# Kernel optimization log

Hardware: AMD Instinct MI355X
Metric: run time of the kernel (lower is better)

Reference implementation:

```python
import jax, jax.numpy as jnp
import numpy as np

# ---- static config (matches init_kwargs cfg) ----
N_IMGS, C_FEAT = 9, 24
HF, WF = 112, 112            # quarter-res feature map
H_IMG, W_IMG = 448, 448      # CDR.IMG_SIZE
HD, WD = 56, 56              # DEPTH_PRED_SIZE
N_PLANES = 64                # DEPTH_MVS.N_INTERVALS
DEPTH_START, DEPTH_INTERVAL = 0.5, 0.05
EDGES_PER_REF = 8
N_EDGES = N_IMGS * EDGES_PER_REF
N_PIX = HD * WD


def setup_inputs() -> dict:
    key = jax.random.key(0)
    k1, k2, k3, k4 = jax.random.split(key, 4)
    feats_quarter = jax.random.normal(k1, (N_IMGS, C_FEAT, HF, WF), jnp.float32)
    # proper rotation matrices via QR so the camera math is well conditioned
    A = jax.random.normal(k2, (N_IMGS, 3, 3), jnp.float32)
    rotmats, _ = jnp.linalg.qr(A)
    rotmats = rotmats.astype(jnp.float32)
    tvecs = 0.1 * jax.random.normal(k3, (N_IMGS, 3), jnp.float32)
    K = jnp.broadcast_to(
        jnp.array([[400.0, 0.0, (W_IMG - 1) / 2.0],
                   [0.0, 400.0, (H_IMG - 1) / 2.0],
                   [0.0, 0.0, 1.0]], jnp.float32), (N_IMGS, 3, 3))
    # ref index sorted+repeated so unique(return_inverse) == ref row itself
    ref = jnp.repeat(jnp.arange(N_IMGS, dtype=jnp.int32), EDGES_PER_REF)
    src = jax.random.randint(k4, (N_EDGES,), 0, N_IMGS, dtype=jnp.int32)
    ref_src_edges = jnp.stack([ref, src], 0)
    return {"feats_quarter": feats_quarter, "rotmats": rotmats,
            "tvecs": tvecs, "K": K, "ref_src_edges": ref_src_edges}


def _forward(feats_quarter, rotmats, tvecs, K, ref_src_edges):
    ref_e, src_e = ref_src_edges[0], ref_src_edges[1]

    # ---- batched_build_plane_sweep_volume_tensor: world-space points per ref view ----
    us = jnp.linspace(0.0, W_IMG - 1.0, WD)
    vs = jnp.linspace(0.0, H_IMG - 1.0, HD)
    uu, vv = jnp.meshgrid(us, vs)                              # [HD, WD]
    pix = jnp.stack([uu, vv, jnp.ones_like(uu)], 0).reshape(3, N_PIX)
    rays = jnp.einsum('nij,jp->nip', jnp.linalg.inv(K), pix)  # [N, 3, P]
    depths = DEPTH_START + DEPTH_INTERVAL * jnp.arange(N_PLANES, dtype=jnp.float32)
    pts_cam = rays[:, None] * depths[None, :, None, None]      # [N, D, 3, P] (plane-major)
    pts_cam = pts_cam.transpose(0, 2, 1, 3).reshape(N_IMGS, 3, N_PLANES * N_PIX)
    pts_world = jnp.einsum('nji,njp->nip', rotmats, pts_cam - tvecs[:, :, None])
    n_pts = N_PLANES * N_PIX

    # ---- project ref-volume points into each src view (per edge) ----
    pts_homo = jnp.concatenate([pts_world, jnp.ones((N_IMGS, 1, n_pts), jnp.float32)], 1)
    P = jnp.einsum('nij,njk->nik', K, jnp.concatenate([rotmats, tvecs[:, :, None]], 2))  # [N,3,4]
    proj = jnp.einsum('eij,ejp->eip', P[src_e], pts_homo[ref_e])  # [E, 3, n_pts]
    z = jnp.abs(proj[:, 2]) + 1e-8
    gx = proj[:, 0] / z / (W_IMG - 1.0) * 2.0 - 1.0
    gy = proj[:, 1] / z / (H_IMG - 1.0) * 2.0 - 1.0

    # ---- bilinear grid_sample, align_corners=True, zeros padding ----
    def sample_one(img, gx1, gy1):  # img [C,HF,WF], gx1/gy1 [n_pts]
        x = (gx1 + 1.0) * 0.5 * (WF - 1)
        y = (gy1 + 1.0) * 0.5 * (HF - 1)
        x0 = jnp.floor(x)
        y0 = jnp.floor(y)
        wx1 = x - x0
        wy1 = y - y0

        def tap(xi, yi, w):
            valid = (xi >= 0) & (xi <= WF - 1) & (yi >= 0) & (yi <= HF - 1)
            xc = jnp.clip(xi, 0, WF - 1).astype(jnp.int32)
            yc = jnp.clip(yi, 0, HF - 1).astype(jnp.int32)
            return jnp.where(valid, w, 0.0)[None] * img[:, yc, xc]  # [C, n_pts]

        return (tap(x0, y0, (1 - wx1) * (1 - wy1))
                + tap(x0 + 1, y0, wx1 * (1 - wy1))
                + tap(x0, y0 + 1, (1 - wx1) * wy1)
                + tap(x0 + 1, y0 + 1, wx1 * wy1))

    x_vox = jax.vmap(sample_one)(feats_quarter[src_e], gx, gy)   # [E, C, n_pts]
    x_vox = x_vox.reshape(N_EDGES, C_FEAT, N_PLANES, HD, WD)

    # ---- scatter mean / sq-mean over edges sharing a ref image, then variance ----
    counts = jax.ops.segment_sum(jnp.ones((N_EDGES,), jnp.float32), ref_e, num_segments=N_IMGS)
    denom = jnp.maximum(counts, 1.0)[:, None, None, None, None]
    x_avg = jax.ops.segment_sum(x_vox, ref_e, num_segments=N_IMGS) / denom
    x_avg_sq = jax.ops.segment_sum(x_vox ** 2, ref_e, num_segments=N_IMGS) / denom
    return x_avg_sq - x_avg ** 2  # [n_ref, C, D, HD, WD]


def reference(feats_quarter, rotmats, tvecs, K, ref_src_edges):
    return _forward(feats_quarter, rotmats, tvecs, K, ref_src_edges)
```

## Files before the change

### kernel.cpp

```cpp
#include <hip/hip_runtime.h>

constexpr int kNImgs   = 9;
constexpr int kC       = 24;
constexpr int kHF      = 112, kWF = 112;
constexpr int kHD      = 56,  kWD = 56;
constexpr int kNPix    = kHD * kWD;
constexpr int kNPlanes = 64;
constexpr int kPtsPerRef = kNPlanes * kNPix;
constexpr int kEdgesPerRef = 8;
constexpr int kNEdges  = kNImgs * kEdgesPerRef;
constexpr int kFeatPix = kHF * kWF;
constexpr int kFeatPerImg = kC * kFeatPix;

constexpr int kDTile = 32, kPTile = 16;
constexpr int kDHalves = kNPlanes / kDTile;
constexpr int kPGroups = kNPix / kPTile;
constexpr int kBlocksPerRef = kDHalves * kPGroups;

typedef _Float16 half8  __attribute__((ext_vector_type(8)));
typedef _Float16 half2v __attribute__((ext_vector_type(2)));

#if __has_builtin(__builtin_amdgcn_fdot2)
__device__ inline float fdot2(half2v a, half2v b, float c) {
  return __builtin_amdgcn_fdot2(a, b, c, false);
}
#else
__device__ inline float fdot2(half2v a, half2v b, float c) {
  return c + (float)a[0] * (float)b[0] + (float)a[1] * (float)b[1];
}
#endif

__device__ inline void mm3(const float* A, const float* B, float* C) {
#pragma unroll
  for (int i = 0; i < 3; ++i)
#pragma unroll
    for (int j = 0; j < 3; ++j)
      C[i*3+j] = A[i*3+0]*B[0*3+j] + A[i*3+1]*B[1*3+j] + A[i*3+2]*B[2*3+j];
}

__device__ inline void inv3(const float* A, float* I) {
  float a=A[0],b=A[1],c=A[2],d=A[3],e=A[4],f=A[5],g=A[6],h=A[7],i=A[8];
  float c00 = e*i - f*h;
  float c01 = -(d*i - f*g);
  float c02 = d*h - e*g;
  float det = a*c00 + b*c01 + c*c02;
  float r = 1.0f / det;
  I[0] = c00*r;           I[1] = (c*h - b*i)*r;  I[2] = (b*f - c*e)*r;
  I[3] = c01*r;           I[4] = (a*i - c*g)*r;  I[5] = (c*d - a*f)*r;
  I[6] = c02*r;           I[7] = (b*g - a*h)*r;  I[8] = (a*e - b*d)*r;
}

__global__ __launch_bounds__(256)
void transpose_feats_kernel(const float* __restrict__ f, _Float16* __restrict__ ft) {
  int idx = blockIdx.x * 256 + threadIdx.x;
  if (idx >= kNImgs * kFeatPerImg) return;
  int n  = idx / kFeatPerImg;
  int r  = idx - n * kFeatPerImg;
  int c  = r / kFeatPix;
  int yx = r - c * kFeatPix;
  ft[((size_t)n * kFeatPix + yx) * kC + c] = (_Float16)f[idx];
}

template <bool TR>
__global__ __launch_bounds__(512)
void psv_var_kernel(const float* __restrict__ feats,
                    const _Float16* __restrict__ featsT,
                    const float* __restrict__ rotmats,
                    const float* __restrict__ tvecs,
                    const float* __restrict__ Kmat,
                    const int*   __restrict__ edges,
                    float* __restrict__ out) {
  __shared__ float sM[kEdgesPerRef][9];
  __shared__ float sB[kEdgesPerRef][3];
  __shared__ int   sSrc[kEdgesPerRef];
  __shared__ int   sUIdx[kEdgesPerRef];
  __shared__ float sMult[kEdgesPerRef];
  __shared__ int   sKU;
  __shared__ float sT[4][kDTile][kPTile + 1];

  const int nwg = gridDim.x;
  const int orig = blockIdx.x;
  const int q = nwg >> 3, r8 = nwg & 7;
  const int xcd = orig & 7, lin = orig >> 3;
  const int bid = ((xcd < r8) ? xcd * (q + 1) : r8 * (q + 1) + (xcd - r8) * q) + lin;

  const int n     = bid / kBlocksPerRef;
  const int rem   = bid - n * kBlocksPerRef;
  const int dHalf = rem / kPGroups;
  const int pG    = rem - dHalf * kPGroups;

  const int t = threadIdx.x;

  if (t < kEdgesPerRef) {
    const int e  = n * kEdgesPerRef + t;
    const int re = edges[e];
    const int se = edges[kNEdges + e];
    sSrc[t] = se;

    const float* Rr = rotmats + re * 9;
    const float* Rs = rotmats + se * 9;
    const float* Kr = Kmat + re * 9;
    const float* Ks = Kmat + se * 9;
    const float* tr = tvecs + re * 3;
    const float* ts = tvecs + se * 3;

    float RrT[9];
#pragma unroll
    for (int i = 0; i < 3; ++i)
#pragma unroll
      for (int j = 0; j < 3; ++j) RrT[i*3+j] = Rr[j*3+i];

    float Kinv[9], A[9], T1[9], M[9];
    inv3(Kr, Kinv);
    mm3(Rs, RrT, A);
    mm3(A, Kinv, T1);
    mm3(Ks, T1, M);

    float At0 = A[0]*tr[0] + A[1]*tr[1] + A[2]*tr[2];
    float At1 = A[3]*tr[0] + A[4]*tr[1] + A[5]*tr[2];
    float At2 = A[6]*tr[0] + A[7]*tr[1] + A[8]*tr[2];
    float bv0 = ts[0] - At0, bv1 = ts[1] - At1, bv2 = ts[2] - At2;
#pragma unroll
    for (int i = 0; i < 9; ++i) sM[t][i] = M[i];
#pragma unroll
    for (int i = 0; i < 3; ++i)
      sB[t][i] = Ks[i*3+0]*bv0 + Ks[i*3+1]*bv1 + Ks[i*3+2]*bv2;
  }
  __syncthreads();

  if (t == 0) {
    int k = 0;
    for (int j = 0; j < kEdgesPerRef; ++j) {
      const int s = sSrc[j];
      bool dup = false;
      for (int i = 0; i < k; ++i) {
        if (sSrc[sUIdx[i]] == s) { sMult[i] += 1.0f; dup = true; break; }
      }
      if (!dup) { sUIdx[k] = j; sMult[k] = 1.0f; ++k; }
    }
    sKU = k;
  }
  __syncthreads();

  const int dsub = t & 31;
  const int psub = t >> 5;
  const int d = dHalf * kDTile + dsub;
  const int p = pG * kPTile + psub;
  const int h = p / kWD;
  const int w = p - h * kWD;

  const float u = (float)w * (447.0f / 55.0f);
  const float v = (float)h * (447.0f / 55.0f);
  const float depth = 0.5f + 0.05f * (float)d;

  float acc[kC], accsq[kC];
#pragma unroll
  for (int c = 0; c < kC; ++c) { acc[c] = 0.0f; accsq[c] = 0.0f; }

  const int kU = sKU;
#pragma unroll 2
  for (int jj = 0; jj < kU; ++jj) {
    const int j = sUIdx[jj];
    const float mult = sMult[jj];
    const float* M = sM[j];
    const float px = depth * (M[0]*u + M[1]*v + M[2]) + sB[j][0];
    const float py = depth * (M[3]*u + M[4]*v + M[5]) + sB[j][1];
    const float pz = depth * (M[6]*u + M[7]*v + M[8]) + sB[j][2];
    const float rz = 1.0f / (fabsf(pz) + 1e-8f);

    const float x = px * rz * (111.0f / 447.0f);
    const float y = py * rz * (111.0f / 447.0f);

    const float x0 = floorf(x), y0 = floorf(y);
    const float wx = x - x0, wy = y - y0;
    const bool vx0 = (x0 >= 0.0f)  && (x0 <= 111.0f);
    const bool vx1 = (x0 >= -1.0f) && (x0 <= 110.0f);
    const bool vy0 = (y0 >= 0.0f)  && (y0 <= 111.0f);
    const bool vy1 = (y0 >= -1.0f) && (y0 <= 110.0f);
    const float w00 = (vx0 && vy0) ? (1.0f - wx) * (1.0f - wy) : 0.0f;
    const float w01 = (vx1 && vy0) ? wx * (1.0f - wy) : 0.0f;
    const float w10 = (vx0 && vy1) ? (1.0f - wx) * wy : 0.0f;
    const float w11 = (vx1 && vy1) ? wx * wy : 0.0f;

    const int xc0 = (int)fminf(fmaxf(x0,        0.0f), 111.0f);
    const int xc1 = (int)fminf(fmaxf(x0 + 1.0f, 0.0f), 111.0f);
    const int yc0 = (int)fminf(fmaxf(y0,        0.0f), 111.0f);
    const int yc1 = (int)fminf(fmaxf(y0 + 1.0f, 0.0f), 111.0f);

    const int src = sSrc[j];
    if constexpr (TR) {
      const half2v wr0 = {(_Float16)w00, (_Float16)w01};
      const half2v wr1 = {(_Float16)w10, (_Float16)w11};
      const _Float16* base = featsT + (size_t)src * kFeatPix * kC;
      const int o00 = (yc0 * kWF + xc0) * kC;
      const int o01 = (yc0 * kWF + xc1) * kC;
      const int o10 = (yc1 * kWF + xc0) * kC;
      const int o11 = (yc1 * kWF + xc1) * kC;
#pragma unroll
      for (int i = 0; i < kC / 8; ++i) {
        const half8 f00 = *(const half8*)(base + o00 + 8*i);
        const half8 f01 = *(const half8*)(base + o01 + 8*i);
        const half8 f10 = *(const half8*)(base + o10 + 8*i);
        const half8 f11 = *(const half8*)(base + o11 + 8*i);
#pragma unroll
        for (int k = 0; k < 8; ++k) {
          const half2v a0 = {f00[k], f01[k]};
          const half2v a1 = {f10[k], f11[k]};
          const float val = fdot2(a1, wr1, fdot2(a0, wr0, 0.0f));
          const int c = 8*i + k;
          const float mval = mult * val;
          acc[c] += mval;
          accsq[c] = __builtin_fmaf(mval, val, accsq[c]);
        }
      }
    } else {
      const float* base = feats + (size_t)src * kFeatPerImg;
      const int o00 = yc0 * kWF + xc0;
      const int o01 = yc0 * kWF + xc1;
      const int o10 = yc1 * kWF + xc0;
      const int o11 = yc1 * kWF + xc1;
#pragma unroll
      for (int c = 0; c < kC; ++c) {
        const float* bc = base + c * kFeatPix;
        float val = w00*bc[o00] + w01*bc[o01] + w10*bc[o10] + w11*bc[o11];
        const float mval = mult * val;
        acc[c] += mval;
        accsq[c] = __builtin_fmaf(mval, val, accsq[c]);
      }
    }
  }

  const int pp2 = t & (kPTile - 1);
  const int dd2 = t >> 4;
  const size_t outBase = (size_t)n * kC * (size_t)kPtsPerRef;
#pragma unroll
  for (int ch = 0; ch < kC / 4; ++ch) {
    __syncthreads();
#pragma unroll
    for (int cc = 0; cc < 4; ++cc) {
      const int c = ch * 4 + cc;
      const float mean = acc[c] * 0.125f;
      const float msq  = accsq[c] * 0.125f;
      sT[cc][dsub][psub] = msq - mean * mean;
    }
    __syncthreads();
#pragma unroll
    for (int cc = 0; cc < 4; ++cc) {
      const int c = ch * 4 + cc;
      out[outBase + ((size_t)c * kNPlanes + (dHalf * kDTile + dd2)) * kNPix
          + pG * kPTile + pp2] = sT[cc][dd2][pp2];
    }
  }
}

extern "C" void kernel_launch(void* const* d_in, const int* in_sizes, int n_in,
                              void* d_out, int out_size, void* d_ws, size_t ws_size,
                              hipStream_t stream) {
  const float* feats  = (const float*)d_in[0];
  const float* rot    = (const float*)d_in[1];
  const float* tv     = (const float*)d_in[2];
  const float* Kmat   = (const float*)d_in[3];
  const int*   edges  = (const int*)d_in[4];
  float* out = (float*)d_out;

  const size_t featsTBytes = (size_t)kNImgs * kFeatPix * kC * sizeof(_Float16);
  const int gridMain = kNImgs * kBlocksPerRef;

  if (ws_size >= featsTBytes) {
    _Float16* featsT = (_Float16*)d_ws;
    const int nT = kNImgs * kFeatPerImg;
    transpose_feats_kernel<<<(nT + 255) / 256, 256, 0, stream>>>(feats, featsT);
    psv_var_kernel<true><<<gridMain, 512, 0, stream>>>(feats, featsT, rot, tv, Kmat, edges, out);
  } else {
    psv_var_kernel<false><<<gridMain, 512, 0, stream>>>(feats, nullptr, rot, tv, Kmat, edges, out);
  }
}
```

Measured before the change: 155.7 us.

## Process both depth halves per thread with packed float2 accumulators

Each block now covers all 64 depth planes for its pixel group: every thread handles two depths (d and d+32). This halves the grid and reuses the per-edge projection terms (M·[u,v,1]) across both depths. Accumulators become float2 vectors so the mean and squared-mean updates can use packed FP32 ops, and the shared transpose tile is re-laid out to [p][d]. The cost is double the accumulator registers (96 floats), which may lower occupancy, plus fewer blocks to spread across the GPU.

Measured after the change: 191.2 us. 1.23x slower.

```diff
diff --git a/kernel.cpp b/kernel.cpp
--- a/kernel.cpp
+++ b/kernel.cpp
@@ -13,12 +13,12 @@
 constexpr int kFeatPerImg = kC * kFeatPix;
 
 constexpr int kDTile = 32, kPTile = 16;
-constexpr int kDHalves = kNPlanes / kDTile;
 constexpr int kPGroups = kNPix / kPTile;
-constexpr int kBlocksPerRef = kDHalves * kPGroups;
+constexpr int kBlocksPerRef = kPGroups;
 
 typedef _Float16 half8  __attribute__((ext_vector_type(8)));
 typedef _Float16 half2v __attribute__((ext_vector_type(2)));
+typedef float    float2v __attribute__((ext_vector_type(2)));
 
 #if __has_builtin(__builtin_amdgcn_fdot2)
 __device__ inline float fdot2(half2v a, half2v b, float c) {
@@ -76,7 +76,7 @@
   __shared__ int   sUIdx[kEdgesPerRef];
   __shared__ float sMult[kEdgesPerRef];
   __shared__ int   sKU;
-  __shared__ float sT[4][kDTile][kPTile + 1];
+  __shared__ float sT[4][kPTile][kDTile + 2];
 
   const int nwg = gridDim.x;
   const int orig = blockIdx.x;
@@ -84,10 +84,8 @@
   const int xcd = orig & 7, lin = orig >> 3;
   const int bid = ((xcd < r8) ? xcd * (q + 1) : r8 * (q + 1) + (xcd - r8) * q) + lin;
 
-  const int n     = bid / kBlocksPerRef;
-  const int rem   = bid - n * kBlocksPerRef;
-  const int dHalf = rem / kPGroups;
-  const int pG    = rem - dHalf * kPGroups;
+  const int n  = bid / kBlocksPerRef;
+  const int pG = bid - n * kBlocksPerRef;
 
   const int t = threadIdx.x;
 
@@ -144,88 +142,112 @@
 
   const int dsub = t & 31;
   const int psub = t >> 5;
-  const int d = dHalf * kDTile + dsub;
   const int p = pG * kPTile + psub;
   const int h = p / kWD;
   const int w = p - h * kWD;
 
   const float u = (float)w * (447.0f / 55.0f);
   const float v = (float)h * (447.0f / 55.0f);
-  const float depth = 0.5f + 0.05f * (float)d;
-
-  float acc[kC], accsq[kC];
-#pragma unroll
-  for (int c = 0; c < kC; ++c) { acc[c] = 0.0f; accsq[c] = 0.0f; }
+  const float depthA = 0.5f + 0.05f * (float)dsub;
+  const float depthB = 0.5f + 0.05f * (float)(dsub + 32);
+
+  float2v acc2[2][kC / 2], accsq2[2][kC / 2];
+#pragma unroll
+  for (int dd = 0; dd < 2; ++dd)
+#pragma unroll
+    for (int i = 0; i < kC / 2; ++i) {
+      acc2[dd][i] = (float2v){0.0f, 0.0f};
+      accsq2[dd][i] = (float2v){0.0f, 0.0f};
+    }
 
   const int kU = sKU;
-#pragma unroll 2
+
   for (int jj = 0; jj < kU; ++jj) {
     const int j = sUIdx[jj];
     const float mult = sMult[jj];
     const float* M = sM[j];
-    const float px = depth * (M[0]*u + M[1]*v + M[2]) + sB[j][0];
-    const float py = depth * (M[3]*u + M[4]*v + M[5]) + sB[j][1];
-    const float pz = depth * (M[6]*u + M[7]*v + M[8]) + sB[j][2];
-    const float rz = 1.0f / (fabsf(pz) + 1e-8f);
-
-    const float x = px * rz * (111.0f / 447.0f);
-    const float y = py * rz * (111.0f / 447.0f);
-
-    const float x0 = floorf(x), y0 = floorf(y);
-    const float wx = x - x0, wy = y - y0;
-    const bool vx0 = (x0 >= 0.0f)  && (x0 <= 111.0f);
-    const bool vx1 = (x0 >= -1.0f) && (x0 <= 110.0f);
-    const bool vy0 = (y0 >= 0.0f)  && (y0 <= 111.0f);
-    const bool vy1 = (y0 >= -1.0f) && (y0 <= 110.0f);
-    const float w00 = (vx0 && vy0) ? (1.0f - wx) * (1.0f - wy) : 0.0f;
-    const float w01 = (vx1 && vy0) ? wx * (1.0f - wy) : 0.0f;
-    const float w10 = (vx0 && vy1) ? (1.0f - wx) * wy : 0.0f;
-    const float w11 = (vx1 && vy1) ? wx * wy : 0.0f;
-
-    const int xc0 = (int)fminf(fmaxf(x0,        0.0f), 111.0f);
-    const int xc1 = (int)fminf(fmaxf(x0 + 1.0f, 0.0f), 111.0f);
-    const int yc0 = (int)fminf(fmaxf(y0,        0.0f), 111.0f);
-    const int yc1 = (int)fminf(fmaxf(y0 + 1.0f, 0.0f), 111.0f);
-
+    const float t0 = M[0]*u + M[1]*v + M[2];
+    const float t1 = M[3]*u + M[4]*v + M[5];
+    const float t2 = M[6]*u + M[7]*v + M[8];
+    const float b0 = sB[j][0], b1 = sB[j][1], b2 = sB[j][2];
     const int src = sSrc[j];
-    if constexpr (TR) {
-      const half2v wr0 = {(_Float16)w00, (_Float16)w01};
-      const half2v wr1 = {(_Float16)w10, (_Float16)w11};
-      const _Float16* base = featsT + (size_t)src * kFeatPix * kC;
-      const int o00 = (yc0 * kWF + xc0) * kC;
-      const int o01 = (yc0 * kWF + xc1) * kC;
-      const int o10 = (yc1 * kWF + xc0) * kC;
-      const int o11 = (yc1 * kWF + xc1) * kC;
-#pragma unroll
-      for (int i = 0; i < kC / 8; ++i) {
-        const half8 f00 = *(const half8*)(base + o00 + 8*i);
-        const half8 f01 = *(const half8*)(base + o01 + 8*i);
-        const half8 f10 = *(const half8*)(base + o10 + 8*i);
-        const half8 f11 = *(const half8*)(base + o11 + 8*i);
-#pragma unroll
-        for (int k = 0; k < 8; ++k) {
-          const half2v a0 = {f00[k], f01[k]};
-          const half2v a1 = {f10[k], f11[k]};
-          const float val = fdot2(a1, wr1, fdot2(a0, wr0, 0.0f));
-          const int c = 8*i + k;
-          const float mval = mult * val;
-          acc[c] += mval;
-          accsq[c] = __builtin_fmaf(mval, val, accsq[c]);
+
+#pragma unroll
+    for (int dd = 0; dd < 2; ++dd) {
+      const float depth = dd ? depthB : depthA;
+      const float px = depth * t0 + b0;
+      const float py = depth * t1 + b1;
+      const float pz = depth * t2 + b2;
+      const float rz = 1.0f / (fabsf(pz) + 1e-8f);
+
+      const float x = px * rz * (111.0f / 447.0f);
+      const float y = py * rz * (111.0f / 447.0f);
+
+      const float x0 = floorf(x), y0 = floorf(y);
+      const float wx = x - x0, wy = y - y0;
+      const bool vx0 = (x0 >= 0.0f)  && (x0 <= 111.0f);
+      const bool vx1 = (x0 >= -1.0f) && (x0 <= 110.0f);
+      const bool vy0 = (y0 >= 0.0f)  && (y0 <= 111.0f);
+      const bool vy1 = (y0 >= -1.0f) && (y0 <= 110.0f);
+      const float w00 = (vx0 && vy0) ? (1.0f - wx) * (1.0f - wy) : 0.0f;
+      const float w01 = (vx1 && vy0) ? wx * (1.0f - wy) : 0.0f;
+      const float w10 = (vx0 && vy1) ? (1.0f - wx) * wy : 0.0f;
+      const float w11 = (vx1 && vy1) ? wx * wy : 0.0f;
+
+      const int xc0 = (int)fminf(fmaxf(x0,        0.0f), 111.0f);
+      const int xc1 = (int)fminf(fmaxf(x0 + 1.0f, 0.0f), 111.0f);
+      const int yc0 = (int)fminf(fmaxf(y0,        0.0f), 111.0f);
+      const int yc1 = (int)fminf(fmaxf(y0 + 1.0f, 0.0f), 111.0f);
+
+      if constexpr (TR) {
+        const half2v wr0 = {(_Float16)w00, (_Float16)w01};
+        const half2v wr1 = {(_Float16)w10, (_Float16)w11};
+        const float2v mult2 = {mult, mult};
+        const _Float16* base = featsT + (size_t)src * kFeatPix * kC;
+        const int o00 = (yc0 * kWF + xc0) * kC;
+        const int o01 = (yc0 * kWF + xc1) * kC;
+        const int o10 = (yc1 * kWF + xc0) * kC;
+        const int o11 = (yc1 * kWF + xc1) * kC;
+#pragma unroll
+        for (int i = 0; i < kC / 8; ++i) {
+          const half8 f00 = *(const half8*)(base + o00 + 8*i);
+          const half8 f01 = *(const half8*)(base + o01 + 8*i);
+          const half8 f10 = *(const half8*)(base + o10 + 8*i);
+          const half8 f11 = *(const half8*)(base + o11 + 8*i);
+#pragma unroll
+          for (int k2 = 0; k2 < 4; ++k2) {
+            const int k0 = 2*k2, k1 = 2*k2 + 1;
+            const half2v a00 = {f00[k0], f01[k0]};
+            const half2v a10 = {f10[k0], f11[k0]};
+            const half2v a01 = {f00[k1], f01[k1]};
+            const half2v a11 = {f10[k1], f11[k1]};
+            const float v0 = fdot2(a10, wr1, fdot2(a00, wr0, 0.0f));
+            const float v1 = fdot2(a11, wr1, fdot2(a01, wr0, 0.0f));
+            const float2v val2 = {v0, v1};
+            const float2v mval2 = mult2 * val2;
+            const int idx = i*4 + k2;
+            acc2[dd][idx] += mval2;
+            accsq2[dd][idx] = mval2 * val2 + accsq2[dd][idx];
+          }
         }
-      }
-    } else {
-      const float* base = feats + (size_t)src * kFeatPerImg;
-      const int o00 = yc0 * kWF + xc0;
-      const int o01 = yc0 * kWF + xc1;
-      const int o10 = yc1 * kWF + xc0;
-      const int o11 = yc1 * kWF + xc1;
-#pragma unroll
-      for (int c = 0; c < kC; ++c) {
-        const float* bc = base + c * kFeatPix;
-        float val = w00*bc[o00] + w01*bc[o01] + w10*bc[o10] + w11*bc[o11];
-        const float mval = mult * val;
-        acc[c] += mval;
-        accsq[c] = __builtin_fmaf(mval, val, accsq[c]);
+      } else {
+        const float* base = feats + (size_t)src * kFeatPerImg;
+        const int o00 = yc0 * kWF + xc0;
+        const int o01 = yc0 * kWF + xc1;
+        const int o10 = yc1 * kWF + xc0;
+        const int o11 = yc1 * kWF + xc1;
+#pragma unroll
+        for (int i = 0; i < kC / 2; ++i) {
+#pragma unroll
+          for (int kk = 0; kk < 2; ++kk) {
+            const int c = 2*i + kk;
+            const float* bc = base + (size_t)c * kFeatPix;
+            float val = w00*bc[o00] + w01*bc[o01] + w10*bc[o10] + w11*bc[o11];
+            const float mval = mult * val;
+            acc2[dd][i][kk] += mval;
+            accsq2[dd][i][kk] = __builtin_fmaf(mval, val, accsq2[dd][i][kk]);
+          }
+        }
       }
     }
   }
@@ -234,21 +256,25 @@
   const int dd2 = t >> 4;
   const size_t outBase = (size_t)n * kC * (size_t)kPtsPerRef;
 #pragma unroll
-  for (int ch = 0; ch < kC / 4; ++ch) {
-    __syncthreads();
-#pragma unroll
-    for (int cc = 0; cc < 4; ++cc) {
-      const int c = ch * 4 + cc;
-      const float mean = acc[c] * 0.125f;
-      const float msq  = accsq[c] * 0.125f;
-      sT[cc][dsub][psub] = msq - mean * mean;
-    }
-    __syncthreads();
-#pragma unroll
-    for (int cc = 0; cc < 4; ++cc) {
-      const int c = ch * 4 + cc;
-      out[outBase + ((size_t)c * kNPlanes + (dHalf * kDTile + dd2)) * kNPix
-          + pG * kPTile + pp2] = sT[cc][dd2][pp2];
+  for (int dd = 0; dd < 2; ++dd) {
+#pragma unroll
+    for (int ch = 0; ch < kC / 4; ++ch) {
+      __syncthreads();
+#pragma unroll
+      for (int cc = 0; cc < 4; ++cc) {
+        const int c = ch * 4 + cc;
+        const float a = acc2[dd][c >> 1][c & 1];
+        const float s = accsq2[dd][c >> 1][c & 1];
+        const float mean = a * 0.125f;
+        sT[cc][psub][dsub] = s * 0.125f - mean * mean;
+      }
+      __syncthreads();
+#pragma unroll
+      for (int cc = 0; cc < 4; ++cc) {
+        const int c = ch * 4 + cc;
+        out[outBase + ((size_t)c * kNPlanes + (dd * kDTile + dd2)) * kNPix
+            + pG * kPTile + pp2] = sT[cc][pp2][dd2];
+      }
     }
   }
 }
```
